# Kernel tuning notes

Hardware: AMD Instinct MI355X
Metric: run time of the kernel (lower is better)

The kernel has to match this reference:

```python
import jax, jax.numpy as jnp
import numpy as np

# Dimensions (match init_kwargs / input_specs)
B, C, H, W = 4, 64, 96, 96
G = 4                # groups of the deformable conv
K = 3                # kernel size
PAD, STRIDE, DIL = 1, 1, 1
KK = K * K


def setup_inputs() -> dict:
    key = jax.random.key(0)
    k1, k2, k3, k4 = jax.random.split(key, 4)
    x = jax.random.normal(k1, (B, C, H, W), jnp.float32)
    # offset-predicting conv: Conv2d(C -> 2*K*K, 3x3), kaiming-ish scale
    w_off = jax.random.normal(k2, (2 * KK, C, K, K), jnp.float32) / np.sqrt(C * KK)
    b_off = jax.random.normal(k3, (2 * KK,), jnp.float32) * 0.01
    # deformable conv weight: [C_out=C, C_in/groups, K, K], bias=False
    w_def = jax.random.normal(k4, (C, C // G, K, K), jnp.float32) / np.sqrt((C // G) * KK)
    return {"x": x, "w_off": w_off, "b_off": b_off, "w_def": w_def}


def _offset_conv(x, w, b):
    y = jax.lax.conv_general_dilated(
        x, w,
        window_strides=(STRIDE, STRIDE),
        padding=((PAD, PAD), (PAD, PAD)),
        rhs_dilation=(DIL, DIL),
        dimension_numbers=("NCHW", "OIHW", "NCHW"))
    return y + b[None, :, None, None]


def _deform_conv2d(x, offset, w_def):
    """torchvision.ops.DeformConv2d (mask=None, bias=None) semantics.

    x:      [B, C, H, W]
    offset: [B, 2*K*K, Ho, Wo]  channel layout (dy_k, dx_k) per kernel tap k=ki*K+kj
    w_def:  [C_out, C_in//G, K, K]
    """
    Bb, Cc, Hh, Ww = x.shape
    Ho, Wo = offset.shape[2], offset.shape[3]
    off = offset.reshape(Bb, KK, 2, Ho, Wo)  # [..., 0]=dy, [..., 1]=dx

    # Base sampling grid per kernel tap: p0 + p_k  -> [KK, Ho, Wo]
    taps = jnp.arange(K, dtype=jnp.float32) * DIL
    base_y = jnp.arange(Ho, dtype=jnp.float32) * STRIDE - PAD  # [Ho]
    base_x = jnp.arange(Wo, dtype=jnp.float32) * STRIDE - PAD  # [Wo]
    gy = (taps[:, None, None, None] + base_y[None, None, :, None])  # [K,1,Ho,1]
    gx = (taps[None, :, None, None] + base_x[None, None, None, :])  # [1,K,1,Wo]
    gy = jnp.broadcast_to(gy, (K, K, Ho, Wo)).reshape(KK, Ho, Wo)
    gx = jnp.broadcast_to(gx, (K, K, Ho, Wo)).reshape(KK, Ho, Wo)

    ys = gy[None] + off[:, :, 0]  # [B, KK, Ho, Wo]
    xs = gx[None] + off[:, :, 1]

    y0 = jnp.floor(ys)
    x0 = jnp.floor(xs)
    wy1 = ys - y0
    wx1 = xs - x0
    wy0 = 1.0 - wy1
    wx0 = 1.0 - wx1
    y0i = y0.astype(jnp.int32)
    x0i = x0.astype(jnp.int32)

    x_flat = x.reshape(Bb, Cc, Hh * Ww)

    def corner(iy, ix, wgt):
        # zero padding outside the image: mask invalid corners
        valid = (iy >= 0) & (iy < Hh) & (ix >= 0) & (ix < Ww)
        idx = jnp.clip(iy, 0, Hh - 1) * Ww + jnp.clip(ix, 0, Ww - 1)  # [B,KK,Ho,Wo]
        g = jnp.take_along_axis(x_flat, idx.reshape(Bb, -1)[:, None, :], axis=2)
        g = g.reshape(Bb, Cc, KK, Ho, Wo)
        return g * (wgt * valid)[:, None]  # broadcast over channels

    sampled = (corner(y0i,     x0i,     wy0 * wx0)
             + corner(y0i,     x0i + 1, wy0 * wx1)
             + corner(y0i + 1, x0i,     wy1 * wx0)
             + corner(y0i + 1, x0i + 1, wy1 * wx1))  # [B,C,KK,Ho,Wo]

    # grouped 9-tap contraction
    s = sampled.reshape(Bb, G, Cc // G, KK, Ho, Wo)
    wv = w_def.reshape(G, w_def.shape[0] // G, Cc // G, KK)  # [G, out/g, in/g, KK]
    out = jnp.einsum("bgckhw,gdck->bgdhw", s, wv)
    return out.reshape(Bb, w_def.shape[0], Ho, Wo)


def reference(x, w_off, b_off, w_def):
    offset = _offset_conv(x, w_off, b_off)
    return _deform_conv2d(x, offset, w_def)
```

## Files before the change

kernel.cpp:

```cpp
#include <hip/hip_runtime.h>
#include <hip/hip_bf16.h>

#define Bn   4
#define Cn   64
#define Hn   96
#define Wn   96
#define Gn   4
#define CGn  16
#define KKn  9
#define NOFF 18
#define HWn  (Hn*Wn)
#define PW   98
#define XH_PIX (PW*PW)
#define PLANE_B (XH_PIX * CGn * 2)

#define OFF_BASE  0
#define AWF_BASE  (Bn*HWn*NOFF)
#define WMF_BASE  (AWF_BASE + 9216)
#define XGH_BASE  (WMF_BASE + 5120)

typedef __attribute__((ext_vector_type(8))) short short8v;
typedef __attribute__((ext_vector_type(4))) float f32x4;
typedef __attribute__((ext_vector_type(2))) float f32x2;
typedef __attribute__((ext_vector_type(4))) unsigned int uint4v;
typedef unsigned short ushort_t;

__device__ inline short f2bs(float v) {
    __hip_bfloat16 h = __float2bfloat16(v);
    return *reinterpret_cast<short*>(&h);
}
__device__ inline unsigned pack2bf(float lo, float hi) {
    return (unsigned)(ushort_t)f2bs(lo) | ((unsigned)(ushort_t)f2bs(hi) << 16);
}

#define NTRB (Bn * (HWn / 64))
#define NHALO (Bn * Gn * 388)
__global__ __launch_bounds__(256) void prep_all(
    const float* __restrict__ x, const float* __restrict__ w_off,
    const float* __restrict__ w_def, float* __restrict__ ws)
{
    __shared__ float t[64][65];
    if (blockIdx.x < NTRB) {
        const int nb = HWn / 64;
        const int b  = blockIdx.x / nb;
        const int p0 = (blockIdx.x % nb) * 64;
        ushort_t* xgh = (ushort_t*)(ws + XGH_BASE);
        for (int i = threadIdx.x; i < 64 * 64; i += 256) {
            const int c = i >> 6, l = i & 63;
            t[c][l] = x[(b * Cn + c) * HWn + p0 + l];
        }
        __syncthreads();
        for (int i = threadIdx.x; i < 64 * 32; i += 256) {
            const int l = i >> 5, cp = i & 31;
            const int pos = p0 + l;
            const int ho = pos / Wn, wo = pos % Wn;
            const unsigned pk = pack2bf(t[cp * 2][l], t[cp * 2 + 1][l]);
            const int g = cp >> 3, pg = cp & 7;
            *(unsigned*)(xgh + ((size_t)(b * Gn + g) * XH_PIX
                                + (ho + 1) * PW + (wo + 1)) * CGn + pg * 2) = pk;
        }
        return;
    }
    const int i = (blockIdx.x - NTRB) * 256 + threadIdx.x;
    const int NA = 18 * 2 * 16 * 4 * 8;
    const int NW = Gn * 5 * CGn * 4 * 8;
    if (i < NA) {
        const int jj  = i & 7;
        const int q   = (i >> 3) & 3;
        const int row = (i >> 5) & 15;
        const int tt  = (i >> 9) & 1;
        const int s   = i >> 10;
        const int u   = s * 4 + q;
        const int k   = u % 9, co = u / 9;
        const int ci  = co * 8 + jj;
        const int o   = tt * 16 + row;
        const float v = (o < NOFF) ? w_off[(o * Cn + ci) * KKn + k] : 0.f;
        ((__hip_bfloat16*)(ws + AWF_BASE))[i] = __float2bfloat16(v);
    } else if (i < NA + NW) {
        const int j  = i - NA;
        const int jj = j & 7;
        const int q  = (j >> 3) & 3;
        const int d  = (j >> 5) & 15;
        const int kp = (j >> 9) % 5;
        const int g  = j / 2560;
        const int c  = (q & 1) * 8 + jj;
        const int k  = 2 * kp + (q >> 1);
        const float v = (k < KKn) ? w_def[((g * CGn + d) * CGn + c) * KKn + k] : 0.f;
        ((__hip_bfloat16*)(ws + WMF_BASE))[j] = __float2bfloat16(v);
    } else {
        const int hidx = i - (NA + NW);
        if (hidx < NHALO) {
            const int plane = hidx / 388;
            const int h = hidx % 388;
            int py, px;
            if (h < 98)       { py = 0;           px = h;        }
            else if (h < 196) { py = 97;          px = h - 98;   }
            else if (h < 292) { py = h - 196 + 1; px = 0;        }
            else              { py = h - 292 + 1; px = 97;       }
            f32x4 z = {0.f, 0.f, 0.f, 0.f};
            f32x4* p = (f32x4*)((ushort_t*)(ws + XGH_BASE)
                       + ((size_t)plane * XH_PIX + py * PW + px) * CGn);
            p[0] = z; p[1] = z;
        }
    }
}

__global__ __launch_bounds__(256) void offset_conv_v4(
    const float* __restrict__ ws, const float* __restrict__ bias,
    float* __restrict__ offs)
{
    const int bid = (blockIdx.x & 7) * 72 + (blockIdx.x >> 3);
    const int b = bid / 144;
    const int r = bid % 144;
    const int wave = threadIdx.x >> 6;
    const int lane = threadIdx.x & 63;
    const int pr = lane & 15, q = lane >> 4;
    const int pos0 = r * 64 + wave * 16;
    const int pos = pos0 + pr;
    const int ho = pos / Wn, wo = pos % Wn;
    const unsigned basep = (unsigned)(ho * PW + wo) * 32u;

    const ushort_t* xhb = (const ushort_t*)(ws + XGH_BASE)
                        + (size_t)b * Gn * XH_PIX * CGn;
    const ushort_t* awf = (const ushort_t*)(ws + AWF_BASE);
    const unsigned pa = (unsigned)(pr * 64 + q * 16);

    f32x4 bi4 = *(const f32x4*)(bias + q * 4);
    f32x2 bi2 = *(const f32x2*)(bias + 16);
    asm volatile("" : "+v"(bi4));
    asm volatile("" : "+v"(bi2));
    asm volatile("s_waitcnt vmcnt(0)" ::: "memory");
    __builtin_amdgcn_sched_barrier(0);

    short8v bfr[6], a0f[6], a1f[6];
    int kk = q, co = 0;
    f32x4 acc0 = {0.f,0.f,0.f,0.f}, acc1 = {0.f,0.f,0.f,0.f};

#define OISSUE(S) { \
    const int ki = kk / 3, kj = kk % 3; \
    const unsigned voff = (unsigned)(co >> 1) * (unsigned)PLANE_B + basep \
                        + (unsigned)(ki * PW + kj) * 32u + (unsigned)(co & 1) * 16u; \
    asm volatile("global_load_dwordx4 %0, %1, %2" : "=v"(bfr[(S)%6]) : "v"(voff), "s"(xhb)); \
    const unsigned aoff = pa + (unsigned)(S) * 2048u; \
    asm volatile("global_load_dwordx4 %0, %1, %2" : "=v"(a0f[(S)%6]) : "v"(aoff), "s"(awf)); \
    asm volatile("global_load_dwordx4 %0, %1, %2" : "=v"(a1f[(S)%6]) : "v"(aoff + 1024u), "s"(awf)); \
    kk += 4; const int cy_ = (kk >= 9) ? 1 : 0; co += cy_; kk -= cy_ * 9; }

#define OCONS(S, N) { \
    asm volatile("s_waitcnt vmcnt(" #N ")" ::: "memory"); \
    __builtin_amdgcn_sched_barrier(0); \
    acc0 = __builtin_amdgcn_mfma_f32_16x16x32_bf16(a0f[(S)%6], bfr[(S)%6], acc0, 0, 0, 0); \
    acc1 = __builtin_amdgcn_mfma_f32_16x16x32_bf16(a1f[(S)%6], bfr[(S)%6], acc1, 0, 0, 0); }

    OISSUE(0) OISSUE(1) OISSUE(2) OISSUE(3) OISSUE(4) OISSUE(5)
    OCONS(0, 15) OISSUE(6)
    OCONS(1, 15) OISSUE(7)
    OCONS(2, 15) OISSUE(8)
    OCONS(3, 15) OISSUE(9)
    OCONS(4, 15) OISSUE(10)
    OCONS(5, 15) OISSUE(11)
    OCONS(6, 15) OISSUE(12)
    OCONS(7, 15) OISSUE(13)
    OCONS(8, 15) OISSUE(14)
    OCONS(9, 15) OISSUE(15)
    OCONS(10, 15) OISSUE(16)
    OCONS(11, 15) OISSUE(17)
    OCONS(12, 15)
    OCONS(13, 12)
    OCONS(14, 9)
    OCONS(15, 6)
    OCONS(16, 3)
    OCONS(17, 0)
#undef OISSUE
#undef OCONS

    float* dst = offs + (size_t)(b * HWn + pos0 + pr) * NOFF + q * 4;
    f32x2 s01; s01.x = acc0[0] + bi4.x; s01.y = acc0[1] + bi4.y;
    f32x2 s23; s23.x = acc0[2] + bi4.z; s23.y = acc0[3] + bi4.w;
    *(f32x2*)dst = s01;
    *(f32x2*)(dst + 2) = s23;
    if (q == 0) {
        f32x2 s67; s67.x = acc1[0] + bi2.x; s67.y = acc1[1] + bi2.y;
        *(f32x2*)(offs + (size_t)(b * HWn + pos0 + pr) * NOFF + 16) = s67;
    }
}

#define GLOAD4(dst, off_) \
    asm volatile("global_load_dwordx4 %0, %1, %2" \
                 : "=v"(dst) : "v"(off_), "s"(xgb))

__global__ __launch_bounds__(256) void deform_v12(
    const float* __restrict__ ws, float* __restrict__ out)
{
    const float* __restrict__ off2 = ws + OFF_BASE;
    const short8v* __restrict__ wmf = (const short8v*)(ws + WMF_BASE);

    const int bid = (blockIdx.x & 7) * 288 + (blockIdx.x >> 3);
    const int nbb = HWn / 64;
    const int bg  = bid / nbb;
    const int g   = bg & (Gn - 1);
    const int b   = bg >> 2;
    const int wave = threadIdx.x >> 6;
    const int lane = threadIdx.x & 63;
    const int pr   = lane & 15;
    const int q    = lane >> 4;
    const int half = q & 1;
    const int tp   = q >> 1;
    const int pos0 = (bid % nbb) * 64 + wave * 16;
    const int pos  = pos0 + pr;
    const int ho = pos / Wn, wo = pos % Wn;

    const f32x2* op2 = (const f32x2*)(off2 + (size_t)(b * HWn + pos) * NOFF);
    f32x2 o2[5];
    #pragma unroll
    for (int kp = 0; kp < 5; kp++) {
        int kq = 2 * kp + tp; if (kq > 8) kq = 8;
        o2[kp] = op2[kq];
    }
    short8v a[5];
    #pragma unroll
    for (int kp = 0; kp < 5; kp++)
        a[kp] = wmf[((g * 5 + kp) * CGn + pr) * 4 + q];

    const ushort_t* xgb = (const ushort_t*)(ws + XGH_BASE)
                        + (size_t)(b * Gn + g) * XH_PIX * CGn;
    const unsigned hoff = (unsigned)half * 16u;

    #pragma unroll
    for (int kp = 0; kp < 5; kp++) {
        asm volatile("" : "+v"(o2[kp]));
        asm volatile("" : "+v"(a[kp]));
    }
    asm volatile("s_waitcnt vmcnt(0)" ::: "memory");
    __builtin_amdgcn_sched_barrier(0);

    float cwt[3][4];
    f32x4 dat[3][4];

#define PAIRSETUP(KP)                                                      \
  {                                                                        \
    const int k  = 2 * (KP) + tp;                                          \
    const int ki = k / 3, kj = k - 3 * ki;                                 \
    const float m = (k <= 8) ? 1.f : 0.f;                                  \
    const float ysf = (float)(ho - 1 + ki) + o2[KP].x;                     \
    const float xsf = (float)(wo - 1 + kj) + o2[KP].y;                     \
    const float y0f = floorf(ysf), x0f = floorf(xsf);                      \
    const int   y0  = (int)y0f,    x0  = (int)x0f;                         \
    const float wy1 = ysf - y0f, wx1 = xsf - x0f;                          \
    const float wy0 = 1.f - wy1, wx0 = 1.f - wx1;                          \
    const bool vy0 = (y0 >= 0)  && (y0 < Hn);                              \
    const bool vy1 = (y0 >= -1) && (y0 < Hn - 1);                          \
    const bool vx0 = (x0 >= 0)  && (x0 < Wn);                              \
    const bool vx1 = (x0 >= -1) && (x0 < Wn - 1);                          \
    const int cy0 = min(max(y0,     0), Hn - 1);                           \
    const int cy1 = min(max(y0 + 1, 0), Hn - 1);                           \
    const int cx0 = min(max(x0,     0), Wn - 1);                           \
    const int cx1 = min(max(x0 + 1, 0), Wn - 1);                           \
    cwt[(KP)%3][0] = m * wy0 * wx0 * ((vy0 && vx0) ? 1.f : 0.f);           \
    cwt[(KP)%3][1] = m * wy0 * wx1 * ((vy0 && vx1) ? 1.f : 0.f);           \
    cwt[(KP)%3][2] = m * wy1 * wx0 * ((vy1 && vx0) ? 1.f : 0.f);           \
    cwt[(KP)%3][3] = m * wy1 * wx1 * ((vy1 && vx1) ? 1.f : 0.f);           \
    const unsigned v00 = (unsigned)((cy0 + 1) * PW + cx0 + 1) * 32u + hoff; \
    const unsigned v01 = (unsigned)((cy0 + 1) * PW + cx1 + 1) * 32u + hoff; \
    const unsigned v10 = (unsigned)((cy1 + 1) * PW + cx0 + 1) * 32u + hoff; \
    const unsigned v11 = (unsigned)((cy1 + 1) * PW + cx1 + 1) * 32u + hoff; \
    GLOAD4(dat[(KP)%3][0], v00);                                           \
    GLOAD4(dat[(KP)%3][1], v01);                                           \
    GLOAD4(dat[(KP)%3][2], v10);                                           \
    GLOAD4(dat[(KP)%3][3], v11);                                           \
  }

    PAIRSETUP(0); PAIRSETUP(1); PAIRSETUP(2);

    f32x4 acc = {0.f, 0.f, 0.f, 0.f};

    #pragma unroll
    for (int kp = 0; kp < 5; kp++) {
        if (kp <= 2)      asm volatile("s_waitcnt vmcnt(8)" ::: "memory");
        else if (kp == 3) asm volatile("s_waitcnt vmcnt(4)" ::: "memory");
        else              asm volatile("s_waitcnt vmcnt(0)" ::: "memory");
        __builtin_amdgcn_sched_barrier(0);

        const int sl = kp % 3;
        float s[8] = {0.f,0.f,0.f,0.f,0.f,0.f,0.f,0.f};
        #pragma unroll
        for (int c4 = 0; c4 < 4; c4++) {
            const float w = cwt[sl][c4];
            const uint4v u = *reinterpret_cast<const uint4v*>(&dat[sl][c4]);
            #pragma unroll
            for (int w2 = 0; w2 < 4; w2++) {
                unsigned lo = u[w2] << 16;
                unsigned hi = u[w2] & 0xffff0000u;
                s[2*w2]   += w * *reinterpret_cast<float*>(&lo);
                s[2*w2+1] += w * *reinterpret_cast<float*>(&hi);
            }
        }
        short8v fr;
        #pragma unroll
        for (int j = 0; j < 8; j++) fr[j] = f2bs(s[j]);
        acc = __builtin_amdgcn_mfma_f32_16x16x32_bf16(a[kp], fr, acc, 0, 0, 0);

        if (kp == 0) { __builtin_amdgcn_sched_barrier(0); PAIRSETUP(3); }
        if (kp == 1) { __builtin_amdgcn_sched_barrier(0); PAIRSETUP(4); }
    }

    float* op = out + (size_t)(b * Cn + g * CGn) * HWn + pos0;
    #pragma unroll
    for (int r = 0; r < 4; r++)
        op[(q * 4 + r) * HWn + pr] = acc[r];
}

extern "C" void kernel_launch(void* const* d_in, const int* in_sizes, int n_in,
                              void* d_out, int out_size, void* d_ws, size_t ws_size,
                              hipStream_t stream) {
    const float* x     = (const float*)d_in[0];
    const float* w_off = (const float*)d_in[1];
    const float* b_off = (const float*)d_in[2];
    const float* w_def = (const float*)d_in[3];
    float* out = (float*)d_out;
    float* ws  = (float*)d_ws;

    const int n_rest = 18432 + 10240 + NHALO;
    const int nblk = NTRB + (n_rest + 255) / 256;
    prep_all<<<nblk, 256, 0, stream>>>(x, w_off, w_def, ws);

    offset_conv_v4<<<576, 256, 0, stream>>>(ws, b_off, ws + OFF_BASE);

    deform_v12<<<Bn * Gn * (HWn / 64), 256, 0, stream>>>(ws, out);
}
```

Measured before the change: 37.25 us.

## Split deformable conv tap pairs across two waves with LDS reduction

Each 16-pixel tile is now handled by two waves: one covers tap pairs 0-2 and the other pairs 3-4, and their MFMA partial sums are combined through shared memory before the store. The block covers 32 positions instead of 64, so twice as many blocks launch. The goal is a shorter serial gather-and-MFMA chain per wave and more memory-level parallelism. In exchange it adds a barrier and an LDS round trip, and the second wave wastes work on a padded, masked sixth pair.

```diff
diff --git a/kernel.cpp b/kernel.cpp
--- a/kernel.cpp
+++ b/kernel.cpp
@@ -189,14 +189,15 @@
     asm volatile("global_load_dwordx4 %0, %1, %2" \
                  : "=v"(dst) : "v"(off_), "s"(xgb))
 
-__global__ __launch_bounds__(256) void deform_v12(
+__global__ __launch_bounds__(256) void deform_v13(
     const float* __restrict__ ws, float* __restrict__ out)
 {
+    __shared__ float red[2][16][16];
     const float* __restrict__ off2 = ws + OFF_BASE;
     const short8v* __restrict__ wmf = (const short8v*)(ws + WMF_BASE);
 
-    const int bid = (blockIdx.x & 7) * 288 + (blockIdx.x >> 3);
-    const int nbb = HWn / 64;
+    const int bid = (blockIdx.x & 7) * 576 + (blockIdx.x >> 3);
+    const int nbb = HWn / 32;
     const int bg  = bid / nbb;
     const int g   = bg & (Gn - 1);
     const int b   = bg >> 2;
@@ -206,30 +207,34 @@
     const int q    = lane >> 4;
     const int half = q & 1;
     const int tp   = q >> 1;
-    const int pos0 = (bid % nbb) * 64 + wave * 16;
+    const int half_t = wave >> 1;
+    const int lo     = wave & 1;
+    const int pos0 = (bid % nbb) * 32 + half_t * 16;
     const int pos  = pos0 + pr;
     const int ho = pos / Wn, wo = pos % Wn;
 
     const f32x2* op2 = (const f32x2*)(off2 + (size_t)(b * HWn + pos) * NOFF);
-    f32x2 o2[5];
+    f32x2 o2[3];
     #pragma unroll
-    for (int kp = 0; kp < 5; kp++) {
-        int kq = 2 * kp + tp; if (kq > 8) kq = 8;
-        o2[kp] = op2[kq];
-    }
-    short8v a[5];
+    for (int i = 0; i < 3; i++) {
+        int kq = 2 * (lo * 3 + i) + tp; if (kq > 8) kq = 8;
+        o2[i] = op2[kq];
+    }
+    short8v a[3];
     #pragma unroll
-    for (int kp = 0; kp < 5; kp++)
-        a[kp] = wmf[((g * 5 + kp) * CGn + pr) * 4 + q];
+    for (int i = 0; i < 3; i++) {
+        int kpa = lo * 3 + i; if (kpa > 4) kpa = 4;
+        a[i] = wmf[((g * 5 + kpa) * CGn + pr) * 4 + q];
+    }
 
     const ushort_t* xgb = (const ushort_t*)(ws + XGH_BASE)
                         + (size_t)(b * Gn + g) * XH_PIX * CGn;
     const unsigned hoff = (unsigned)half * 16u;
 
     #pragma unroll
-    for (int kp = 0; kp < 5; kp++) {
-        asm volatile("" : "+v"(o2[kp]));
-        asm volatile("" : "+v"(a[kp]));
+    for (int i = 0; i < 3; i++) {
+        asm volatile("" : "+v"(o2[i]));
+        asm volatile("" : "+v"(a[i]));
     }
     asm volatile("s_waitcnt vmcnt(0)" ::: "memory");
     __builtin_amdgcn_sched_barrier(0);
@@ -237,13 +242,14 @@
     float cwt[3][4];
     f32x4 dat[3][4];
 
-#define PAIRSETUP(KP)                                                      \
+#define PAIRSETUP(I)                                                       \
   {                                                                        \
-    const int k  = 2 * (KP) + tp;                                          \
-    const int ki = k / 3, kj = k - 3 * ki;                                 \
+    const int k  = 2 * (lo * 3 + (I)) + tp;                                \
+    const int kc = (k > 8) ? 8 : k;                                        \
+    const int ki = kc / 3, kj = kc - 3 * ki;                               \
     const float m = (k <= 8) ? 1.f : 0.f;                                  \
-    const float ysf = (float)(ho - 1 + ki) + o2[KP].x;                     \
-    const float xsf = (float)(wo - 1 + kj) + o2[KP].y;                     \
+    const float ysf = (float)(ho - 1 + ki) + o2[I].x;                      \
+    const float xsf = (float)(wo - 1 + kj) + o2[I].y;                      \
     const float y0f = floorf(ysf), x0f = floorf(xsf);                      \
     const int   y0  = (int)y0f,    x0  = (int)x0f;                         \
     const float wy1 = ysf - y0f, wx1 = xsf - x0f;                          \
@@ -256,18 +262,18 @@
     const int cy1 = min(max(y0 + 1, 0), Hn - 1);                           \
     const int cx0 = min(max(x0,     0), Wn - 1);                           \
     const int cx1 = min(max(x0 + 1, 0), Wn - 1);                           \
-    cwt[(KP)%3][0] = m * wy0 * wx0 * ((vy0 && vx0) ? 1.f : 0.f);           \
-    cwt[(KP)%3][1] = m * wy0 * wx1 * ((vy0 && vx1) ? 1.f : 0.f);           \
-    cwt[(KP)%3][2] = m * wy1 * wx0 * ((vy1 && vx0) ? 1.f : 0.f);           \
-    cwt[(KP)%3][3] = m * wy1 * wx1 * ((vy1 && vx1) ? 1.f : 0.f);           \
+    cwt[I][0] = m * wy0 * wx0 * ((vy0 && vx0) ? 1.f : 0.f);                \
+    cwt[I][1] = m * wy0 * wx1 * ((vy0 && vx1) ? 1.f : 0.f);                \
+    cwt[I][2] = m * wy1 * wx0 * ((vy1 && vx0) ? 1.f : 0.f);                \
+    cwt[I][3] = m * wy1 * wx1 * ((vy1 && vx1) ? 1.f : 0.f);                \
     const unsigned v00 = (unsigned)((cy0 + 1) * PW + cx0 + 1) * 32u + hoff; \
     const unsigned v01 = (unsigned)((cy0 + 1) * PW + cx1 + 1) * 32u + hoff; \
     const unsigned v10 = (unsigned)((cy1 + 1) * PW + cx0 + 1) * 32u + hoff; \
     const unsigned v11 = (unsigned)((cy1 + 1) * PW + cx1 + 1) * 32u + hoff; \
-    GLOAD4(dat[(KP)%3][0], v00);                                           \
-    GLOAD4(dat[(KP)%3][1], v01);                                           \
-    GLOAD4(dat[(KP)%3][2], v10);                                           \
-    GLOAD4(dat[(KP)%3][3], v11);                                           \
+    GLOAD4(dat[I][0], v00);                                                \
+    GLOAD4(dat[I][1], v01);                                                \
+    GLOAD4(dat[I][2], v10);                                                \
+    GLOAD4(dat[I][3], v11);                                                \
   }
 
     PAIRSETUP(0); PAIRSETUP(1); PAIRSETUP(2);
@@ -275,39 +281,42 @@
     f32x4 acc = {0.f, 0.f, 0.f, 0.f};
 
     #pragma unroll
-    for (int kp = 0; kp < 5; kp++) {
-        if (kp <= 2)      asm volatile("s_waitcnt vmcnt(8)" ::: "memory");
-        else if (kp == 3) asm volatile("s_waitcnt vmcnt(4)" ::: "memory");
-        else              asm volatile("s_waitcnt vmcnt(0)" ::: "memory");
+    for (int i = 0; i < 3; i++) {
+        if (i == 0)      asm volatile("s_waitcnt vmcnt(8)" ::: "memory");
+        else if (i == 1) asm volatile("s_waitcnt vmcnt(4)" ::: "memory");
+        else             asm volatile("s_waitcnt vmcnt(0)" ::: "memory");
         __builtin_amdgcn_sched_barrier(0);
 
-        const int sl = kp % 3;
         float s[8] = {0.f,0.f,0.f,0.f,0.f,0.f,0.f,0.f};
         #pragma unroll
         for (int c4 = 0; c4 < 4; c4++) {
-            const float w = cwt[sl][c4];
-            const uint4v u = *reinterpret_cast<const uint4v*>(&dat[sl][c4]);
+            const float w = cwt[i][c4];
+            const uint4v u = *reinterpret_cast<const uint4v*>(&dat[i][c4]);
             #pragma unroll
             for (int w2 = 0; w2 < 4; w2++) {
-                unsigned lo = u[w2] << 16;
-                unsigned hi = u[w2] & 0xffff0000u;
-                s[2*w2]   += w * *reinterpret_cast<float*>(&lo);
-                s[2*w2+1] += w * *reinterpret_cast<float*>(&hi);
+                unsigned lov = u[w2] << 16;
+                unsigned hiv = u[w2] & 0xffff0000u;
+                s[2*w2]   += w * *reinterpret_cast<float*>(&lov);
+                s[2*w2+1] += w * *reinterpret_cast<float*>(&hiv);
             }
         }
         short8v fr;
         #pragma unroll
         for (int j = 0; j < 8; j++) fr[j] = f2bs(s[j]);
-        acc = __builtin_amdgcn_mfma_f32_16x16x32_bf16(a[kp], fr, acc, 0, 0, 0);
-
-        if (kp == 0) { __builtin_amdgcn_sched_barrier(0); PAIRSETUP(3); }
-        if (kp == 1) { __builtin_amdgcn_sched_barrier(0); PAIRSETUP(4); }
-    }
-
-    float* op = out + (size_t)(b * Cn + g * CGn) * HWn + pos0;
-    #pragma unroll
-    for (int r = 0; r < 4; r++)
-        op[(q * 4 + r) * HWn + pr] = acc[r];
+        acc = __builtin_amdgcn_mfma_f32_16x16x32_bf16(a[i], fr, acc, 0, 0, 0);
+    }
+
+    if (lo == 1) {
+        *(f32x4*)&red[half_t][pr][q * 4] = acc;
+    }
+    __syncthreads();
+    if (lo == 0) {
+        const f32x4 other = *(const f32x4*)&red[half_t][pr][q * 4];
+        float* op = out + (size_t)(b * Cn + g * CGn) * HWn + pos0;
+        #pragma unroll
+        for (int r = 0; r < 4; r++)
+            op[(q * 4 + r) * HWn + pr] = acc[r] + other[r];
+    }
 }
 
 extern "C" void kernel_launch(void* const* d_in, const int* in_sizes, int n_in,
@@ -326,5 +335,5 @@
 
     offset_conv_v4<<<576, 256, 0, stream>>>(ws, b_off, ws + OFF_BASE);
 
-    deform_v12<<<Bn * Gn * (HWn / 64), 256, 0, stream>>>(ws, out);
-}
+    deform_v13<<<Bn * Gn * (HWn / 32), 256, 0, stream>>>(ws, out);
+}
```

Result: slower. 39.91 us (+7.1%).
